# Kernel optimization log

Measured on AMD Instinct MI355X. Metric: run time of the kernel, lower is better.

Reference implementation:

```python
import jax, jax.numpy as jnp
import numpy as np

NUM_EXPERTS = 64
TOP_K = 8
NUM_TOKENS = 8192
HIDDEN = 1024
INTER = 512


def setup_inputs() -> dict:
    key = jax.random.key(0)
    k1, k2, k3, k4 = jax.random.split(key, 4)
    # 0.02 scale keeps activations in a sane range (randn weights with fan-in 1024)
    return {
        "hidden_states": jax.random.normal(k1, (NUM_TOKENS, HIDDEN), jnp.float32),
        "router_weight": jax.random.normal(k2, (HIDDEN, NUM_EXPERTS), jnp.float32) * 0.02,
        "merged_gate_up_proj": jax.random.normal(k3, (NUM_EXPERTS, HIDDEN, 2 * INTER), jnp.float32) * 0.02,
        "merged_down_proj": jax.random.normal(k4, (NUM_EXPERTS, INTER, HIDDEN), jnp.float32) * 0.02,
    }


def reference(hidden_states, router_weight, merged_gate_up_proj, merged_down_proj):
    T, H = hidden_states.shape
    E = router_weight.shape[1]

    # ---- Router: softmax over experts, top-k, renormalize top-k weights ----
    logits = hidden_states @ router_weight                       # [T, E]
    probs = jax.nn.softmax(logits, axis=-1)
    routing_weights, routing_indices = jax.lax.top_k(probs, TOP_K)  # [T, k]
    routing_weights = routing_weights / routing_weights.sum(-1, keepdims=True)

    # ---- Permute (haojun_permute_topk): replicate tokens topk times, stable-sort by expert ----
    flat_indices = routing_indices.reshape(-1)                   # [T*k]
    sort_order = jnp.argsort(flat_indices)                       # stable sort
    flat_states = jnp.repeat(hidden_states, TOP_K, axis=0)       # [T*k, H]
    permuted = flat_states[sort_order]                           # tokens grouped by expert
    group_sizes = jnp.bincount(flat_indices, length=E).astype(jnp.int32)  # tokens per expert

    # ---- Grouped MLP (grouped_gemm.gmm equivalent): y_i = x_i @ W[expert(i)] ----
    merged = jax.lax.ragged_dot(permuted, merged_gate_up_proj, group_sizes)  # [T*k, 2*I]
    gate, up = jnp.split(merged, 2, axis=-1)
    h = jax.nn.silu(gate) * up                                   # SiLU-gated (hidden_act='silu')
    expert_out = jax.lax.ragged_dot(h, merged_down_proj, group_sizes)        # [T*k, H]

    # ---- Unpermute: invert the sort, weight by routing probs, sum over top-k ----
    inv = jnp.argsort(sort_order)                                # unsort_order
    unpermuted = expert_out[inv].reshape(T, TOP_K, H)
    return (unpermuted * routing_weights[..., None]).sum(axis=1)  # [T, H]
```

## Files before the change

### kernel.cpp

```cpp
#include <hip/hip_runtime.h>
#include <cstdint>
#include <cstddef>

typedef __bf16 bf16_t;
typedef __bf16 bf16x8 __attribute__((ext_vector_type(8)));
typedef __bf16 bf16x4 __attribute__((ext_vector_type(4)));
typedef float f32x4 __attribute__((ext_vector_type(4)));

#define T_TOKENS 8192
#define HID 1024
#define INTER 512
#define NEXP 64
#define TOPK 8
#define NROWS (T_TOKENS * TOPK)

typedef const unsigned int __attribute__((address_space(1)))* gptr_t;
typedef unsigned int __attribute__((address_space(3)))* lptr_t;

__device__ __forceinline__ void gload_lds16(const void* g, void* l) {
  __builtin_amdgcn_global_load_lds((gptr_t)g, (lptr_t)l, 16, 0, 0);
}

__device__ __forceinline__ f32x4 mfma16(bf16x8 a, bf16x8 b, f32x4 c) {
  return __builtin_amdgcn_mfma_f32_16x16x32_bf16(a, b, c, 0, 0, 0);
}

__global__ void transpose_cvt_kernel(const float* __restrict__ W, bf16_t* __restrict__ Wt,
                                     int K, int N) {
  const int e = blockIdx.z;
  const int n0 = blockIdx.x * 64, k0 = blockIdx.y * 64;
  const int tid = threadIdx.x;
  __shared__ bf16_t tile[64][65];
  {
    const int r = tid >> 2, cq = tid & 3;
    const float* src = W + ((size_t)e * K + k0 + r) * N + n0 + cq * 16;
#pragma unroll
    for (int q = 0; q < 4; ++q) {
      float4 v = *(const float4*)(src + q * 4);
      tile[r][cq * 16 + q * 4 + 0] = (bf16_t)v.x;
      tile[r][cq * 16 + q * 4 + 1] = (bf16_t)v.y;
      tile[r][cq * 16 + q * 4 + 2] = (bf16_t)v.z;
      tile[r][cq * 16 + q * 4 + 3] = (bf16_t)v.w;
    }
  }
  __syncthreads();
  {
    const int nl = tid >> 2, kq = tid & 3;
    __align__(16) bf16_t tmp[16];
#pragma unroll
    for (int i = 0; i < 16; ++i) tmp[i] = tile[kq * 16 + i][nl];
    bf16_t* dst = Wt + ((size_t)e * N + n0 + nl) * K + k0 + kq * 16;
    *(bf16x8*)(dst + 0) = *(const bf16x8*)(tmp + 0);
    *(bf16x8*)(dst + 8) = *(const bf16x8*)(tmp + 8);
  }
}

__global__ void cvt_bf16_kernel(const float* __restrict__ in, bf16_t* __restrict__ out, int n4) {
  int i = blockIdx.x * blockDim.x + threadIdx.x;
  if (i < n4) {
    float4 v = ((const float4*)in)[i];
    bf16x4 o;
    o[0] = (bf16_t)v.x; o[1] = (bf16_t)v.y; o[2] = (bf16_t)v.z; o[3] = (bf16_t)v.w;
    ((bf16x4*)out)[i] = o;
  }
}

__global__ void router_kernel(const float* __restrict__ hs, const float* __restrict__ rw,
                              float* __restrict__ wval, int* __restrict__ widx) {
  const int t = blockIdx.x;
  const int tid = threadIdx.x;
  const int e = tid & 63, w = tid >> 6;
  const float* hrow = hs + (size_t)t * HID;
  float acc = 0.f;
  const int kbeg = w * (HID / 4);
#pragma unroll 4
  for (int k0 = kbeg; k0 < kbeg + HID / 4; k0 += 4) {
    float4 hv = *(const float4*)(hrow + k0);
    acc = fmaf(hv.x, rw[(size_t)(k0 + 0) * NEXP + e], acc);
    acc = fmaf(hv.y, rw[(size_t)(k0 + 1) * NEXP + e], acc);
    acc = fmaf(hv.z, rw[(size_t)(k0 + 2) * NEXP + e], acc);
    acc = fmaf(hv.w, rw[(size_t)(k0 + 3) * NEXP + e], acc);
  }
  __shared__ float part[4][64];
  part[w][e] = acc;
  __syncthreads();
  if (tid < 64) {
    float logit = part[0][e] + part[1][e] + part[2][e] + part[3][e];
    float m = logit;
    for (int off = 32; off; off >>= 1) m = fmaxf(m, __shfl_xor(m, off));
    float ex = expf(logit - m);
    float Z = ex;
    for (int off = 32; off; off >>= 1) Z += __shfl_xor(Z, off);
    float p = ex / Z;
    float sum8 = 0.f;
    float outv[8]; int outi[8];
#pragma unroll
    for (int s = 0; s < 8; ++s) {
      float v = p; int idx = e;
      for (int off = 32; off; off >>= 1) {
        float vv = __shfl_xor(v, off);
        int ii = __shfl_xor(idx, off);
        if (vv > v || (vv == v && ii < idx)) { v = vv; idx = ii; }
      }
      outv[s] = v; outi[s] = idx; sum8 += v;
      if (e == idx) p = -1.f;
    }
    if (e == 0) {
      float inv = 1.f / sum8;
#pragma unroll
      for (int s = 0; s < 8; ++s) {
        wval[(size_t)t * TOPK + s] = outv[s] * inv;
        widx[(size_t)t * TOPK + s] = outi[s];
      }
    }
  }
}

__global__ void hist_kernel(const int* __restrict__ widx, int* __restrict__ cnt) {
  __shared__ int h[NEXP];
  if (threadIdx.x < NEXP) h[threadIdx.x] = 0;
  __syncthreads();
  for (int i = blockIdx.x * blockDim.x + threadIdx.x; i < NROWS; i += gridDim.x * blockDim.x)
    atomicAdd(&h[widx[i]], 1);
  __syncthreads();
  if (threadIdx.x < NEXP) atomicAdd(&cnt[threadIdx.x], h[threadIdx.x]);
}

__global__ void scan_kernel(const int* __restrict__ cnt, int* __restrict__ seg,
                            int* __restrict__ cnt2) {
  if (threadIdx.x == 0) {
    int a = 0;
    for (int e2 = 0; e2 < NEXP; ++e2) { seg[e2] = a; a += cnt[e2]; }
    seg[NEXP] = a;
  }
  if (threadIdx.x < NEXP) cnt2[threadIdx.x] = 0;
}

__global__ void assign_kernel(const int* __restrict__ widx, const int* __restrict__ seg,
                              int* __restrict__ cnt2, int* __restrict__ row_org) {
  for (int i = blockIdx.x * blockDim.x + threadIdx.x; i < NROWS; i += gridDim.x * blockDim.x) {
    int e = widx[i];
    int p = seg[e] + atomicAdd(&cnt2[e], 1);
    row_org[p] = i;
  }
}

__launch_bounds__(256, 2)
__global__ void gemm1_kernel(const bf16_t* __restrict__ hb, const bf16_t* __restrict__ Wt1,
                             const int* __restrict__ row_org, const int* __restrict__ seg,
                             bf16_t* __restrict__ h) {
  const int e = blockIdx.z;
  const int ms = seg[e];
  const int sz = seg[e + 1] - ms;
  const int n0 = blockIdx.x * 128;
  const int tid = threadIdx.x;
  const int lane = tid & 63;
  const int wid = tid >> 6;
  const int wm = wid >> 1, wn = wid & 1;
  __shared__ __align__(16) bf16_t As[128 * 64];
  __shared__ __align__(16) bf16_t Bs[256 * 64];

  const int srow = tid >> 3;
  const int cg = (tid & 7) ^ (srow & 7);

  size_t boff[8];
#pragma unroll
  for (int b = 0; b < 8; ++b) {
    int brow = b * 32 + srow;
    int n = (brow < 128) ? (n0 + brow) : (512 + n0 + (brow - 128));
    boff[b] = ((size_t)e * 1024 + n) * 1024 + cg * 8;
  }
  const int l15 = lane & 15, l4 = lane >> 4;

  for (int m0 = blockIdx.y * 128; m0 < sz; m0 += 16 * 128) {
    size_t aoff[4];
#pragma unroll
    for (int a = 0; a < 4; ++a) {
      int row = a * 32 + srow;
      int idx = m0 + row; if (idx >= sz) idx = sz - 1;
      aoff[a] = (size_t)(row_org[ms + idx] >> 3) * HID + cg * 8;
    }
    f32x4 accg[4][4], accu[4][4];
#pragma unroll
    for (int mi = 0; mi < 4; ++mi)
#pragma unroll
      for (int ni = 0; ni < 4; ++ni) {
        accg[mi][ni] = (f32x4){0.f, 0.f, 0.f, 0.f};
        accu[mi][ni] = (f32x4){0.f, 0.f, 0.f, 0.f};
      }

    for (int kt = 0; kt < 16; ++kt) {
      const int ko = kt * 64;
      __syncthreads();
#pragma unroll
      for (int a = 0; a < 4; ++a)
        gload_lds16(hb + aoff[a] + ko, (char*)As + a * 4096 + tid * 16);
#pragma unroll
      for (int b = 0; b < 8; ++b)
        gload_lds16(Wt1 + boff[b] + ko, (char*)Bs + b * 4096 + tid * 16);
      __syncthreads();
#pragma unroll
      for (int kf = 0; kf < 2; ++kf) {
        const int ch = kf * 4 + l4;
        bf16x8 af[4], bg[4], bu[4];
#pragma unroll
        for (int mi = 0; mi < 4; ++mi) {
          int r = wm * 64 + mi * 16 + l15;
          af[mi] = *(const bf16x8*)((const char*)As + r * 128 + ((ch ^ (r & 7)) << 4));
        }
#pragma unroll
        for (int ni = 0; ni < 4; ++ni) {
          int rg = wn * 64 + ni * 16 + l15;
          bg[ni] = *(const bf16x8*)((const char*)Bs + rg * 128 + ((ch ^ (rg & 7)) << 4));
          int ru = rg + 128;
          bu[ni] = *(const bf16x8*)((const char*)Bs + ru * 128 + ((ch ^ (ru & 7)) << 4));
        }
#pragma unroll
        for (int mi = 0; mi < 4; ++mi)
#pragma unroll
          for (int ni = 0; ni < 4; ++ni) {
            accg[mi][ni] = mfma16(af[mi], bg[ni], accg[mi][ni]);
            accu[mi][ni] = mfma16(af[mi], bu[ni], accu[mi][ni]);
          }
      }
    }
#pragma unroll
    for (int mi = 0; mi < 4; ++mi) {
#pragma unroll
      for (int j = 0; j < 4; ++j) {
        int mrow = wm * 64 + mi * 16 + l4 * 4 + j;
        int idx = m0 + mrow;
        if (idx < sz) {
          bf16_t* hrow = h + (size_t)(ms + idx) * INTER + n0 + wn * 64 + l15;
#pragma unroll
          for (int ni = 0; ni < 4; ++ni) {
            float g = accg[mi][ni][j];
            float u = accu[mi][ni][j];
            float s = g / (1.f + __expf(-g));
            hrow[ni * 16] = (bf16_t)(s * u);
          }
        }
      }
    }
  }
}

__launch_bounds__(256, 2)
__global__ void gemm2_kernel(const bf16_t* __restrict__ h, const bf16_t* __restrict__ Wt2,
                             const int* __restrict__ row_org, const int* __restrict__ seg,
                             bf16_t* __restrict__ eo) {
  const int e = blockIdx.z;
  const int ms = seg[e];
  const int sz = seg[e + 1] - ms;
  const int n0 = blockIdx.x * 128;
  const int tid = threadIdx.x;
  const int lane = tid & 63;
  const int wid = tid >> 6;
  const int wm = wid >> 1, wn = wid & 1;
  __shared__ __align__(16) bf16_t As[128 * 64];
  __shared__ __align__(16) bf16_t Bs[128 * 64];
  const int srow = tid >> 3;
  const int cg = (tid & 7) ^ (srow & 7);
  size_t boff[4];
#pragma unroll
  for (int b = 0; b < 4; ++b) {
    int brow = b * 32 + srow;
    boff[b] = ((size_t)e * 1024 + n0 + brow) * INTER + cg * 8;
  }
  const int l15 = lane & 15, l4 = lane >> 4;

  for (int m0 = blockIdx.y * 128; m0 < sz; m0 += 16 * 128) {
    size_t aoff[4];
#pragma unroll
    for (int a = 0; a < 4; ++a) {
      int row = a * 32 + srow;
      int idx = m0 + row; if (idx >= sz) idx = sz - 1;
      aoff[a] = (size_t)(ms + idx) * INTER + cg * 8;
    }
    f32x4 acc[4][4];
#pragma unroll
    for (int mi = 0; mi < 4; ++mi)
#pragma unroll
      for (int ni = 0; ni < 4; ++ni) acc[mi][ni] = (f32x4){0.f, 0.f, 0.f, 0.f};

    for (int kt = 0; kt < 8; ++kt) {
      const int ko = kt * 64;
      __syncthreads();
#pragma unroll
      for (int a = 0; a < 4; ++a)
        gload_lds16(h + aoff[a] + ko, (char*)As + a * 4096 + tid * 16);
#pragma unroll
      for (int b = 0; b < 4; ++b)
        gload_lds16(Wt2 + boff[b] + ko, (char*)Bs + b * 4096 + tid * 16);
      __syncthreads();
#pragma unroll
      for (int kf = 0; kf < 2; ++kf) {
        const int ch = kf * 4 + l4;
        bf16x8 af[4], bb[4];
#pragma unroll
        for (int mi = 0; mi < 4; ++mi) {
          int r = wm * 64 + mi * 16 + l15;
          af[mi] = *(const bf16x8*)((const char*)As + r * 128 + ((ch ^ (r & 7)) << 4));
        }
#pragma unroll
        for (int ni = 0; ni < 4; ++ni) {
          int r = wn * 64 + ni * 16 + l15;
          bb[ni] = *(const bf16x8*)((const char*)Bs + r * 128 + ((ch ^ (r & 7)) << 4));
        }
#pragma unroll
        for (int mi = 0; mi < 4; ++mi)
#pragma unroll
          for (int ni = 0; ni < 4; ++ni)
            acc[mi][ni] = mfma16(af[mi], bb[ni], acc[mi][ni]);
      }
    }
#pragma unroll
    for (int mi = 0; mi < 4; ++mi) {
#pragma unroll
      for (int j = 0; j < 4; ++j) {
        int mrow = wm * 64 + mi * 16 + l4 * 4 + j;
        int idx = m0 + mrow;
        if (idx < sz) {
          int org = row_org[ms + idx];
          bf16_t* orow = eo + (size_t)org * HID + n0 + wn * 64 + l15;
#pragma unroll
          for (int ni = 0; ni < 4; ++ni)
            orow[ni * 16] = (bf16_t)acc[mi][ni][j];
        }
      }
    }
  }
}

__global__ void unpermute_kernel(const bf16_t* __restrict__ eo, const float* __restrict__ wval,
                                 float* __restrict__ out) {
  const int t = blockIdx.x;
  const int c0 = threadIdx.x * 4;
  float w[8];
#pragma unroll
  for (int s = 0; s < 8; ++s) w[s] = wval[(size_t)t * 8 + s];
  float acc[4] = {0.f, 0.f, 0.f, 0.f};
#pragma unroll
  for (int s = 0; s < 8; ++s) {
    bf16x4 v = *(const bf16x4*)(eo + ((size_t)t * 8 + s) * HID + c0);
#pragma unroll
    for (int q = 0; q < 4; ++q) acc[q] = fmaf(w[s], (float)v[q], acc[q]);
  }
  *(float4*)(out + (size_t)t * HID + c0) = *(float4*)acc;
}

extern "C" void kernel_launch(void* const* d_in, const int* in_sizes, int n_in,
                              void* d_out, int out_size, void* d_ws, size_t ws_size,
                              hipStream_t stream) {
  (void)in_sizes; (void)n_in; (void)ws_size; (void)out_size;
  const float* hs = (const float*)d_in[0];
  const float* rw = (const float*)d_in[1];
  const float* w1 = (const float*)d_in[2];
  const float* w2 = (const float*)d_in[3];
  float* out = (float*)d_out;

  char* p = (char*)d_ws;
  size_t off = 0;
  auto carve = [&](size_t bytes) {
    void* r = p + off;
    off = (off + bytes + 255) & ~(size_t)255;
    return r;
  };
  bf16_t* Wt1  = (bf16_t*)carve((size_t)NEXP * 1024 * 1024 * 2);
  bf16_t* Wt2  = (bf16_t*)carve((size_t)NEXP * 1024 * 512 * 2);
  bf16_t* hb   = (bf16_t*)carve((size_t)T_TOKENS * HID * 2);
  bf16_t* hmid = (bf16_t*)carve((size_t)NROWS * INTER * 2);
  float* wval  = (float*)carve((size_t)NROWS * 4);
  int* widx    = (int*)carve((size_t)NROWS * 4);
  int* row_org = (int*)carve((size_t)NROWS * 4);
  int* cnt     = (int*)carve(256);
  int* seg     = (int*)carve(66 * 4);
  int* cnt2    = (int*)carve(256);

  bf16_t* eo = Wt1;

  (void)hipMemsetAsync(cnt, 0, 256, stream);

  transpose_cvt_kernel<<<dim3(16, 16, NEXP), 256, 0, stream>>>(w1, Wt1, 1024, 1024);
  transpose_cvt_kernel<<<dim3(16, 8, NEXP), 256, 0, stream>>>(w2, Wt2, 512, 1024);
  cvt_bf16_kernel<<<(T_TOKENS * HID / 4 + 255) / 256, 256, 0, stream>>>(hs, hb, T_TOKENS * HID / 4);
  router_kernel<<<T_TOKENS, 256, 0, stream>>>(hs, rw, wval, widx);
  hist_kernel<<<128, 256, 0, stream>>>(widx, cnt);
  scan_kernel<<<1, 64, 0, stream>>>(cnt, seg, cnt2);
  assign_kernel<<<128, 256, 0, stream>>>(widx, seg, cnt2, row_org);
  gemm1_kernel<<<dim3(4, 16, NEXP), 256, 0, stream>>>(hb, Wt1, row_org, seg, hmid);
  gemm2_kernel<<<dim3(8, 16, NEXP), 256, 0, stream>>>(hmid, Wt2, row_org, seg, eo);
  unpermute_kernel<<<T_TOKENS, 256, 0, stream>>>(eo, wval, out);
}
```

Measured before the change: 678.6 us.

## Batch router tokens, swizzle GEMM blocks across XCDs, widen unpermute and transpose stores

The router now handles 16 tokens per block, staging hidden states in LDS so each router weight load is reused across tokens instead of being reloaded per token. Both grouped GEMMs remap block IDs with an XCD swizzle so blocks of the same expert land on the same XCD for L2 reuse, and their launch bounds rise to 3 waves per SIMD. The unpermute kernel processes 8 columns per thread with 128 threads, and the transpose kernel writes bf16x4 vectors into a padded LDS tile. The higher occupancy target may force register spills in the GEMMs, and the router block's larger LDS footprint limits occupancy.

```diff
diff --git a/kernel.cpp b/kernel.cpp
--- a/kernel.cpp
+++ b/kernel.cpp
@@ -13,6 +13,7 @@
 #define NEXP 64
 #define TOPK 8
 #define NROWS (T_TOKENS * TOPK)
+#define RT_TOK 16
 
 typedef const unsigned int __attribute__((address_space(1)))* gptr_t;
 typedef unsigned int __attribute__((address_space(3)))* lptr_t;
@@ -23,6 +24,12 @@
 
 __device__ __forceinline__ f32x4 mfma16(bf16x8 a, bf16x8 b, f32x4 c) {
   return __builtin_amdgcn_mfma_f32_16x16x32_bf16(a, b, c, 0, 0, 0);
+}
+
+__device__ __forceinline__ int xcd_swizzle(int bid, int nwg) {
+  int q = nwg >> 3;
+  int xcd = bid & 7, i = bid >> 3;
+  return xcd * q + i;
 }
 
 __global__ void transpose_cvt_kernel(const float* __restrict__ W, bf16_t* __restrict__ Wt,
@@ -30,17 +37,16 @@
   const int e = blockIdx.z;
   const int n0 = blockIdx.x * 64, k0 = blockIdx.y * 64;
   const int tid = threadIdx.x;
-  __shared__ bf16_t tile[64][65];
+  __shared__ __align__(8) bf16_t tile[64][68];
   {
     const int r = tid >> 2, cq = tid & 3;
     const float* src = W + ((size_t)e * K + k0 + r) * N + n0 + cq * 16;
 #pragma unroll
     for (int q = 0; q < 4; ++q) {
       float4 v = *(const float4*)(src + q * 4);
-      tile[r][cq * 16 + q * 4 + 0] = (bf16_t)v.x;
-      tile[r][cq * 16 + q * 4 + 1] = (bf16_t)v.y;
-      tile[r][cq * 16 + q * 4 + 2] = (bf16_t)v.z;
-      tile[r][cq * 16 + q * 4 + 3] = (bf16_t)v.w;
+      bf16x4 b;
+      b[0] = (bf16_t)v.x; b[1] = (bf16_t)v.y; b[2] = (bf16_t)v.z; b[3] = (bf16_t)v.w;
+      *(bf16x4*)&tile[r][cq * 16 + q * 4] = b;
     }
   }
   __syncthreads();
@@ -65,27 +71,47 @@
   }
 }
 
+__launch_bounds__(256, 2)
 __global__ void router_kernel(const float* __restrict__ hs, const float* __restrict__ rw,
                               float* __restrict__ wval, int* __restrict__ widx) {
-  const int t = blockIdx.x;
+  const int t0 = blockIdx.x * RT_TOK;
   const int tid = threadIdx.x;
-  const int e = tid & 63, w = tid >> 6;
-  const float* hrow = hs + (size_t)t * HID;
-  float acc = 0.f;
-  const int kbeg = w * (HID / 4);
-#pragma unroll 4
-  for (int k0 = kbeg; k0 < kbeg + HID / 4; k0 += 4) {
-    float4 hv = *(const float4*)(hrow + k0);
-    acc = fmaf(hv.x, rw[(size_t)(k0 + 0) * NEXP + e], acc);
-    acc = fmaf(hv.y, rw[(size_t)(k0 + 1) * NEXP + e], acc);
-    acc = fmaf(hv.z, rw[(size_t)(k0 + 2) * NEXP + e], acc);
-    acc = fmaf(hv.w, rw[(size_t)(k0 + 3) * NEXP + e], acc);
-  }
-  __shared__ float part[4][64];
-  part[w][e] = acc;
+  const int lane = tid & 63, w = tid >> 6;
+  __shared__ float hsl[RT_TOK][HID / 4][4];
+  __shared__ float part[4][RT_TOK][NEXP];
+
+  for (int i = tid; i < RT_TOK * (HID / 4); i += 256) {
+    int t = i >> 8, c = i & 255;
+    *(float4*)&hsl[t][c][0] = ((const float4*)(hs + (size_t)(t0 + t) * HID))[c];
+  }
   __syncthreads();
-  if (tid < 64) {
-    float logit = part[0][e] + part[1][e] + part[2][e] + part[3][e];
+
+  float acc[RT_TOK];
+#pragma unroll
+  for (int t = 0; t < RT_TOK; ++t) acc[t] = 0.f;
+  const int kb = w * 256;
+  for (int kc = 0; kc < 64; ++kc) {
+    const int k = kb + kc * 4;
+    float r0 = rw[(size_t)(k + 0) * NEXP + lane];
+    float r1 = rw[(size_t)(k + 1) * NEXP + lane];
+    float r2 = rw[(size_t)(k + 2) * NEXP + lane];
+    float r3 = rw[(size_t)(k + 3) * NEXP + lane];
+#pragma unroll
+    for (int t = 0; t < RT_TOK; ++t) {
+      float4 hv = *(const float4*)&hsl[t][(kb >> 2) + kc][0];
+      acc[t] = fmaf(hv.x, r0, acc[t]);
+      acc[t] = fmaf(hv.y, r1, acc[t]);
+      acc[t] = fmaf(hv.z, r2, acc[t]);
+      acc[t] = fmaf(hv.w, r3, acc[t]);
+    }
+  }
+#pragma unroll
+  for (int t = 0; t < RT_TOK; ++t) part[w][t][lane] = acc[t];
+  __syncthreads();
+
+  for (int j = 0; j < 4; ++j) {
+    const int t = w * 4 + j;
+    float logit = part[0][t][lane] + part[1][t][lane] + part[2][t][lane] + part[3][t][lane];
     float m = logit;
     for (int off = 32; off; off >>= 1) m = fmaxf(m, __shfl_xor(m, off));
     float ex = expf(logit - m);
@@ -96,21 +122,21 @@
     float outv[8]; int outi[8];
 #pragma unroll
     for (int s = 0; s < 8; ++s) {
-      float v = p; int idx = e;
+      float v = p; int idx = lane;
       for (int off = 32; off; off >>= 1) {
         float vv = __shfl_xor(v, off);
         int ii = __shfl_xor(idx, off);
         if (vv > v || (vv == v && ii < idx)) { v = vv; idx = ii; }
       }
       outv[s] = v; outi[s] = idx; sum8 += v;
-      if (e == idx) p = -1.f;
-    }
-    if (e == 0) {
+      if (lane == idx) p = -1.f;
+    }
+    if (lane == 0) {
       float inv = 1.f / sum8;
 #pragma unroll
       for (int s = 0; s < 8; ++s) {
-        wval[(size_t)t * TOPK + s] = outv[s] * inv;
-        widx[(size_t)t * TOPK + s] = outi[s];
+        wval[(size_t)(t0 + t) * TOPK + s] = outv[s] * inv;
+        widx[(size_t)(t0 + t) * TOPK + s] = outi[s];
       }
     }
   }
@@ -145,14 +171,19 @@
   }
 }
 
-__launch_bounds__(256, 2)
+__launch_bounds__(256, 3)
 __global__ void gemm1_kernel(const bf16_t* __restrict__ hb, const bf16_t* __restrict__ Wt1,
                              const int* __restrict__ row_org, const int* __restrict__ seg,
                              bf16_t* __restrict__ h) {
-  const int e = blockIdx.z;
+  const int bid = blockIdx.x + gridDim.x * (blockIdx.y + gridDim.y * blockIdx.z);
+  const int swz = xcd_swizzle(bid, 16 * 4 * NEXP);
+  const int mt = swz & 15;
+  const int nt = (swz >> 4) & 3;
+  const int e = swz >> 6;
+
   const int ms = seg[e];
   const int sz = seg[e + 1] - ms;
-  const int n0 = blockIdx.x * 128;
+  const int n0 = nt * 128;
   const int tid = threadIdx.x;
   const int lane = tid & 63;
   const int wid = tid >> 6;
@@ -172,7 +203,7 @@
   }
   const int l15 = lane & 15, l4 = lane >> 4;
 
-  for (int m0 = blockIdx.y * 128; m0 < sz; m0 += 16 * 128) {
+  for (int m0 = mt * 128; m0 < sz; m0 += 16 * 128) {
     size_t aoff[4];
 #pragma unroll
     for (int a = 0; a < 4; ++a) {
@@ -245,14 +276,19 @@
   }
 }
 
-__launch_bounds__(256, 2)
+__launch_bounds__(256, 3)
 __global__ void gemm2_kernel(const bf16_t* __restrict__ h, const bf16_t* __restrict__ Wt2,
                              const int* __restrict__ row_org, const int* __restrict__ seg,
                              bf16_t* __restrict__ eo) {
-  const int e = blockIdx.z;
+  const int bid = blockIdx.x + gridDim.x * (blockIdx.y + gridDim.y * blockIdx.z);
+  const int swz = xcd_swizzle(bid, 16 * 8 * NEXP);
+  const int mt = swz & 15;
+  const int nt = (swz >> 4) & 7;
+  const int e = swz >> 7;
+
   const int ms = seg[e];
   const int sz = seg[e + 1] - ms;
-  const int n0 = blockIdx.x * 128;
+  const int n0 = nt * 128;
   const int tid = threadIdx.x;
   const int lane = tid & 63;
   const int wid = tid >> 6;
@@ -269,7 +305,7 @@
   }
   const int l15 = lane & 15, l4 = lane >> 4;
 
-  for (int m0 = blockIdx.y * 128; m0 < sz; m0 += 16 * 128) {
+  for (int m0 = mt * 128; m0 < sz; m0 += 16 * 128) {
     size_t aoff[4];
 #pragma unroll
     for (int a = 0; a < 4; ++a) {
@@ -335,18 +371,19 @@
 __global__ void unpermute_kernel(const bf16_t* __restrict__ eo, const float* __restrict__ wval,
                                  float* __restrict__ out) {
   const int t = blockIdx.x;
-  const int c0 = threadIdx.x * 4;
+  const int c0 = threadIdx.x * 8;
   float w[8];
 #pragma unroll
   for (int s = 0; s < 8; ++s) w[s] = wval[(size_t)t * 8 + s];
-  float acc[4] = {0.f, 0.f, 0.f, 0.f};
+  float acc[8] = {0.f, 0.f, 0.f, 0.f, 0.f, 0.f, 0.f, 0.f};
 #pragma unroll
   for (int s = 0; s < 8; ++s) {
-    bf16x4 v = *(const bf16x4*)(eo + ((size_t)t * 8 + s) * HID + c0);
-#pragma unroll
-    for (int q = 0; q < 4; ++q) acc[q] = fmaf(w[s], (float)v[q], acc[q]);
-  }
-  *(float4*)(out + (size_t)t * HID + c0) = *(float4*)acc;
+    bf16x8 v = *(const bf16x8*)(eo + ((size_t)t * 8 + s) * HID + c0);
+#pragma unroll
+    for (int q = 0; q < 8; ++q) acc[q] = fmaf(w[s], (float)v[q], acc[q]);
+  }
+  *(float4*)(out + (size_t)t * HID + c0) = *(float4*)&acc[0];
+  *(float4*)(out + (size_t)t * HID + c0 + 4) = *(float4*)&acc[4];
 }
 
 extern "C" void kernel_launch(void* const* d_in, const int* in_sizes, int n_in,
@@ -384,11 +421,11 @@
   transpose_cvt_kernel<<<dim3(16, 16, NEXP), 256, 0, stream>>>(w1, Wt1, 1024, 1024);
   transpose_cvt_kernel<<<dim3(16, 8, NEXP), 256, 0, stream>>>(w2, Wt2, 512, 1024);
   cvt_bf16_kernel<<<(T_TOKENS * HID / 4 + 255) / 256, 256, 0, stream>>>(hs, hb, T_TOKENS * HID / 4);
-  router_kernel<<<T_TOKENS, 256, 0, stream>>>(hs, rw, wval, widx);
+  router_kernel<<<T_TOKENS / RT_TOK, 256, 0, stream>>>(hs, rw, wval, widx);
   hist_kernel<<<128, 256, 0, stream>>>(widx, cnt);
   scan_kernel<<<1, 64, 0, stream>>>(cnt, seg, cnt2);
   assign_kernel<<<128, 256, 0, stream>>>(widx, seg, cnt2, row_org);
-  gemm1_kernel<<<dim3(4, 16, NEXP), 256, 0, stream>>>(hb, Wt1, row_org, seg, hmid);
-  gemm2_kernel<<<dim3(8, 16, NEXP), 256, 0, stream>>>(hmid, Wt2, row_org, seg, eo);
-  unpermute_kernel<<<T_TOKENS, 256, 0, stream>>>(eo, wval, out);
-}
+  gemm1_kernel<<<dim3(16, 4, NEXP), 256, 0, stream>>>(hb, Wt1, row_org, seg, hmid);
+  gemm2_kernel<<<dim3(16, 8, NEXP), 256, 0, stream>>>(hmid, Wt2, row_org, seg, eo);
+  unpermute_kernel<<<T_TOKENS, 128, 0, stream>>>(eo, wval, out);
+}
```

Result: slower. 844.0 us (+24.4%).
